# Kernel tuning notes

Measured on AMD Instinct MI355X. Metric: run time of the kernel, lower is better.

The kernel has to match this reference:

```python
import jax, jax.numpy as jnp
import numpy as np

L, B, T, D, H, FF = 4, 8, 1024, 256, 8, 1024
DK = D // H
SCALE = 1.0 / np.sqrt(DK)


def _ln(x, g, b, eps=1e-6):
    m = jnp.mean(x, axis=-1, keepdims=True)
    v = jnp.mean(jnp.square(x - m), axis=-1, keepdims=True)
    return (x - m) * jax.lax.rsqrt(v + eps) * g + b


def _l2norm(x, eps=1e-8):
    n = jnp.sqrt(jnp.sum(jnp.square(x), axis=-1, keepdims=True))
    return x / jnp.maximum(n, eps)


def setup_inputs() -> dict:
    key = jax.random.key(0)
    ks = jax.random.split(key, 8)
    s = 0.02
    inp = {
        'x': jax.random.normal(ks[0], (B, T, D), dtype=jnp.float32),
        'padding_mask': jnp.zeros((B, T), dtype=bool),
        'ln1_g': jnp.ones((L, D), jnp.float32), 'ln1_b': jnp.zeros((L, D), jnp.float32),
        'qn_g': jnp.ones((L, D), jnp.float32), 'qn_b': jnp.zeros((L, D), jnp.float32),
        'Wqkv': jax.random.normal(ks[1], (L, 3 * D, D), jnp.float32) * s,
        'bqkv': jnp.zeros((L, 3 * D), jnp.float32),
        'Wo': jax.random.normal(ks[2], (L, D, D), jnp.float32) * s,
        'bo': jnp.zeros((L, D), jnp.float32),
        'ln2_g': jnp.ones((L, D), jnp.float32), 'ln2_b': jnp.zeros((L, D), jnp.float32),
        'W1': jax.random.normal(ks[3], (L, FF, D), jnp.float32) * s,
        'b1': jnp.zeros((L, FF), jnp.float32),
        'W2': jax.random.normal(ks[4], (L, D, FF), jnp.float32) * s,
        'b2': jnp.zeros((L, D), jnp.float32),
        'alpha': jnp.full((L,), 0.1, jnp.float32),
        'beta': jnp.full((L,), 0.1, jnp.float32),
    }
    return inp


def _block(x, pad_mask, p):
    (g1, bb1, qg, qb, wqkv, bqkv, wo, bo, g2, bb2, w1, b1, w2, b2, a, be) = p
    Bn, Tn, Dn = x.shape
    # --- SemiCausalAttention on norm1(x) ---
    xn = _ln(x, g1, bb1)
    h = _ln(xn, qg, qb)                      # q_norm LayerNorm
    qkv = h @ wqkv.T + bqkv                  # [B,T,3D]
    qkv = qkv.reshape(Bn, Tn, 3, H, DK).transpose(2, 0, 3, 1, 4)  # [3,B,H,T,dk]
    Q, K, V = qkv[0], qkv[1], qkv[2]
    Q = _l2norm(Q)
    K = _l2norm(K)
    scores = jnp.einsum('bhtd,bhsd->bhts', Q, K) * SCALE
    scores = jnp.clip(scores, -10.0, 10.0)
    causal = jnp.triu(jnp.ones((Tn, Tn), dtype=bool), k=1)        # True = future
    scores = jnp.where(causal[None, None], -10000.0, scores)
    scores = jnp.where(pad_mask[:, None, None, :], -10000.0, scores)
    attn = jax.nn.softmax(scores, axis=-1)
    ao = jnp.einsum('bhts,bhsd->bhtd', attn, V)                   # [B,H,T,dk]
    ao = ao.transpose(0, 2, 1, 3).reshape(Bn, Tn, Dn)
    attn_out = (ao @ wo.T + bo) * 0.5
    x = x + jnp.tanh(a) * attn_out
    # --- FFN ---
    f = _ln(x, g2, bb2)
    f = jax.nn.gelu(f @ w1.T + b1, approximate=False)
    f = f @ w2.T + b2
    x = x + jnp.tanh(be) * f
    return jnp.clip(x, -100.0, 100.0)


def reference(x, padding_mask, ln1_g, ln1_b, qn_g, qn_b, Wqkv, bqkv, Wo, bo,
              ln2_g, ln2_b, W1, b1, W2, b2, alpha, beta):
    params = (ln1_g, ln1_b, qn_g, qn_b, Wqkv, bqkv, Wo, bo,
              ln2_g, ln2_b, W1, b1, W2, b2, alpha, beta)

    def step(carry, p):
        return _block(carry, padding_mask, p), None

    out, _ = jax.lax.scan(step, x, params)
    return out
```

## Files before the change

kernel.cpp:

```cpp
#include <hip/hip_runtime.h>
#include <hip/hip_bf16.h>
#include <math.h>

#define BB 8
#define TT 1024
#define DD 256
#define HH 8
#define BT 8192

typedef __attribute__((ext_vector_type(4))) float f32x4;
typedef __attribute__((ext_vector_type(16))) float f32x16;
typedef __attribute__((ext_vector_type(8))) short short8;
typedef __attribute__((ext_vector_type(4))) short short4v;
typedef __attribute__((ext_vector_type(8))) __bf16 bf16x8;

__device__ inline float bf2f(short s) {
  unsigned int u = ((unsigned int)(unsigned short)s) << 16;
  return __builtin_bit_cast(float, u);
}
__device__ inline short f2bf(float f) {
  unsigned int u = __builtin_bit_cast(unsigned int, f);
  unsigned int lsb = (u >> 16) & 1u;
  u += 0x7fffu + lsb;
  return (short)(u >> 16);
}
__device__ inline unsigned int cvtpk(float lo, float hi) {
  unsigned int r;
  asm("v_cvt_pk_bf16_f32 %0, %1, %2" : "=v"(r) : "v"(lo), "v"(hi));
  return r;
}

__device__ inline f32x4 mfma16(short8 a, short8 b, f32x4 c) {
  return __builtin_amdgcn_mfma_f32_16x16x32_bf16(
      __builtin_bit_cast(bf16x8, a), __builtin_bit_cast(bf16x8, b), c, 0, 0, 0);
}
__device__ inline f32x16 mfma32(short8 a, short8 b, f32x16 c) {
  return __builtin_amdgcn_mfma_f32_32x32x16_bf16(
      __builtin_bit_cast(bf16x8, a), __builtin_bit_cast(bf16x8, b), c, 0, 0, 0);
}

__device__ inline void gload_lds16(void* lds, const void* g) {
  __builtin_amdgcn_global_load_lds(
      (const __attribute__((address_space(1))) unsigned int*)g,
      (__attribute__((address_space(3))) unsigned int*)lds, 16, 0, 0);
}

__global__ __launch_bounds__(256) void cvt_all(
    const float4* __restrict__ s0, short4v* __restrict__ d0, int n0,
    const float4* __restrict__ s1, short4v* __restrict__ d1, int n1,
    const float4* __restrict__ s2, short4v* __restrict__ d2, int n2,
    const float4* __restrict__ s3, short4v* __restrict__ d3, int n3)
{
  int i = blockIdx.x * 256 + threadIdx.x;
  const float4* s; short4v* d;
  if (i < n0) { s = s0 + i; d = d0 + i; }
  else if ((i -= n0) < n1) { s = s1 + i; d = d1 + i; }
  else if ((i -= n1) < n2) { s = s2 + i; d = d2 + i; }
  else if ((i -= n2) < n3) { s = s3 + i; d = d3 + i; }
  else return;
  float4 v = *s;
  short4v o;
  o[0] = f2bf(v.x); o[1] = f2bf(v.y); o[2] = f2bf(v.z); o[3] = f2bf(v.w);
  *d = o;
}

__global__ __launch_bounds__(256) void ln_kernel(
    const float* __restrict__ Xin,
    const float* __restrict__ g1, const float* __restrict__ b1,
    const float* __restrict__ g2, const float* __restrict__ b2,
    short* __restrict__ out)
{
  const int row = blockIdx.x * 4 + (threadIdx.x >> 6);
  const int lane = threadIdx.x & 63;
  const float4 v = *(const float4*)(Xin + (size_t)row * 256 + lane * 4);
  float y[4] = {v.x, v.y, v.z, v.w};

  float s = y[0] + y[1] + y[2] + y[3];
  #pragma unroll
  for (int m = 32; m >= 1; m >>= 1) s += __shfl_xor(s, m, 64);
  float mean = s * (1.0f / 256.0f);
  float sq = 0.f;
  #pragma unroll
  for (int i = 0; i < 4; ++i) { y[i] -= mean; sq += y[i] * y[i]; }
  #pragma unroll
  for (int m = 32; m >= 1; m >>= 1) sq += __shfl_xor(sq, m, 64);
  float rs = rsqrtf(sq * (1.0f / 256.0f) + 1e-6f);
  #pragma unroll
  for (int i = 0; i < 4; ++i) y[i] = y[i] * rs * g1[lane * 4 + i] + b1[lane * 4 + i];

  float s2 = y[0] + y[1] + y[2] + y[3];
  #pragma unroll
  for (int m = 32; m >= 1; m >>= 1) s2 += __shfl_xor(s2, m, 64);
  float m2 = s2 * (1.0f / 256.0f);
  float sq2 = 0.f;
  #pragma unroll
  for (int i = 0; i < 4; ++i) { y[i] -= m2; sq2 += y[i] * y[i]; }
  #pragma unroll
  for (int m = 32; m >= 1; m >>= 1) sq2 += __shfl_xor(sq2, m, 64);
  float rs2 = rsqrtf(sq2 * (1.0f / 256.0f) + 1e-6f);
  #pragma unroll
  for (int i = 0; i < 4; ++i) y[i] = y[i] * rs2 * g2[lane * 4 + i] + b2[lane * 4 + i];

  #pragma unroll
  for (int i = 0; i < 4; ++i) out[(size_t)row * 256 + lane * 4 + i] = f2bf(y[i]);
}

template<int BN, int EPI>
__global__ __launch_bounds__(256) void gemm_bt(
    const short* __restrict__ A, const short* __restrict__ Bw,
    const float* __restrict__ bias,
    short* __restrict__ O0, short* __restrict__ O1, short* __restrict__ O2,
    int M, int N, int K)
{
  constexpr int MI = (BN == 128) ? 4 : 2;
  __shared__ __align__(16) short A_s[2][128 * 64];
  __shared__ __align__(16) short B_s[2][BN * 64];
  const int tid = threadIdx.x;
  const int lane = tid & 63;
  const int w = tid >> 6;
  const int lo4 = lane & 15, hi2 = lane >> 4;
  int wm, wn0;
  if (BN == 128) { wm = (w >> 1) * 64; wn0 = (w & 1) * 64; }
  else           { wm = w * 32;        wn0 = 0; }
  const int bid = blockIdx.x + blockIdx.y * gridDim.x;
  const int nwg = gridDim.x * gridDim.y;
  const int wg = (bid & 7) * (nwg >> 3) + (bid >> 3);
  const int tM = (wg / gridDim.x) * 128, tN = (wg % gridDim.x) * BN;

  f32x4 acc[MI][4];
  #pragma unroll
  for (int i = 0; i < MI; ++i)
    #pragma unroll
    for (int j = 0; j < 4; ++j) acc[i][j] = (f32x4){0.f, 0.f, 0.f, 0.f};

  auto stage = [&](int buf, int k0) {
    #pragma unroll
    for (int ri = 0; ri < 4; ++ri) {
      int o = ri * 2048 + tid * 8;
      int row = o >> 6;
      int col = (o & 63) ^ ((row & 7) << 3);
      gload_lds16(&A_s[buf][ri * 2048 + w * 512], A + (size_t)(tM + row) * K + k0 + col);
    }
    #pragma unroll
    for (int ri = 0; ri < BN / 32; ++ri) {
      int o = ri * 2048 + tid * 8;
      int row = o >> 6;
      int col = (o & 63) ^ ((row & 7) << 3);
      gload_lds16(&B_s[buf][ri * 2048 + w * 512], Bw + (size_t)(tN + row) * K + k0 + col);
    }
  };

  const int nt = K >> 6;
  stage(0, 0);
  __syncthreads();
  for (int t = 0; t < nt; ++t) {
    const int cur = t & 1;
    if (t + 1 < nt) stage(cur ^ 1, (t + 1) << 6);
    #pragma unroll
    for (int kc = 0; kc < 2; ++kc) {
      short8 af[MI], bfr[4];
      #pragma unroll
      for (int i = 0; i < MI; ++i) {
        int row = wm + i * 16 + lo4;
        af[i] = *(const short8*)&A_s[cur][row * 64 + ((kc * 32 + hi2 * 8) ^ ((row & 7) << 3))];
      }
      #pragma unroll
      for (int j = 0; j < 4; ++j) {
        int row = wn0 + j * 16 + lo4;
        bfr[j] = *(const short8*)&B_s[cur][row * 64 + ((kc * 32 + hi2 * 8) ^ ((row & 7) << 3))];
      }
      #pragma unroll
      for (int i = 0; i < MI; ++i)
        #pragma unroll
        for (int j = 0; j < 4; ++j)
          acc[i][j] = mfma16(af[i], bfr[j], acc[i][j]);
    }
    __syncthreads();
  }

  if (EPI == 4) {
    #pragma unroll
    for (int i = 0; i < MI; ++i)
      #pragma unroll
      for (int j = 0; j < 4; ++j)
        #pragma unroll
        for (int r = 0; r < 4; ++r)
          acc[i][j][r] += bias[tN + wn0 + j * 16 + lo4];
    if (tN >= 512) {
      #pragma unroll
      for (int i = 0; i < MI; ++i) {
        #pragma unroll
        for (int j = 0; j < 4; ++j) {
          short4v o;
          #pragma unroll
          for (int r = 0; r < 4; ++r) o[r] = f2bf(acc[i][j][r]);
          int row0 = tM + wm + i * 16 + hi2 * 4;
          int colr = (tN + wn0 + j * 16 + lo4) - 512;
          int h = colr >> 5, d = colr & 31;
          int b = row0 >> 10, t0 = row0 & 1023;
          *(short4v*)(O2 + (((size_t)(b * 8 + h) * 32 + d) << 10) + t0) = o;
        }
      }
      return;
    }
    {
      const float C2 = 0.25503489702966368f;
      const float sc = (tN < 256) ? C2 : 1.0f;
      #pragma unroll
      for (int i = 0; i < MI; ++i) {
        #pragma unroll
        for (int r = 0; r < 4; ++r) {
          float s01 = acc[i][0][r] * acc[i][0][r] + acc[i][1][r] * acc[i][1][r];
          float s23 = acc[i][2][r] * acc[i][2][r] + acc[i][3][r] * acc[i][3][r];
          #pragma unroll
          for (int m = 1; m <= 8; m <<= 1) {
            s01 += __shfl_xor(s01, m, 64);
            s23 += __shfl_xor(s23, m, 64);
          }
          float n01 = sc / fmaxf(sqrtf(s01), 1e-8f);
          float n23 = sc / fmaxf(sqrtf(s23), 1e-8f);
          acc[i][0][r] *= n01; acc[i][1][r] *= n01;
          acc[i][2][r] *= n23; acc[i][3][r] *= n23;
        }
      }
    }
    short* dst = (tN < 256) ? O0 : O1;
    #pragma unroll
    for (int i = 0; i < MI; ++i)
      #pragma unroll
      for (int j = 0; j < 4; ++j)
        #pragma unroll
        for (int r = 0; r < 4; ++r) {
          int row = tM + wm + i * 16 + hi2 * 4 + r;
          int colr = (tN + wn0 + j * 16 + lo4) & 255;
          int h = colr >> 5, d = colr & 31;
          size_t idx = (((size_t)((row >> 10) * 8 + h) << 10) | (size_t)(row & 1023)) * 32 + d;
          dst[idx] = f2bf(acc[i][j][r]);
        }
    return;
  }

  #pragma unroll
  for (int i = 0; i < MI; ++i) {
    #pragma unroll
    for (int j = 0; j < 4; ++j) {
      #pragma unroll
      for (int r = 0; r < 4; ++r) {
        int row = tM + wm + i * 16 + hi2 * 4 + r;
        int col = tN + wn0 + j * 16 + lo4;
        float v = acc[i][j][r] + bias[col];
        size_t idx = (size_t)row * N + col;
        if (EPI == 2) {
          float t1 = v * v;
          float arg = fminf(v * (1.0f + 0.044715f * t1) * 2.3022077f, 80.0f);
          float ex;
          asm("v_exp_f32 %0, %1" : "=v"(ex) : "v"(arg));
          float gl = v * ex * __builtin_amdgcn_rcpf(ex + 1.0f);
          O0[idx] = f2bf(gl);
        } else {
          O0[idx] = f2bf(v);
        }
      }
    }
  }
}

template<int MODE>
__global__ __launch_bounds__(256) void gemm_ln(
    const short* __restrict__ A, const short* __restrict__ Bw,
    const float* __restrict__ bias, const float* Xin, float* X,
    short* __restrict__ Obf, const float* __restrict__ scale_p,
    const float* __restrict__ gA, const float* __restrict__ bA,
    const float* __restrict__ gB, const float* __restrict__ bB,
    int K, int doLN)
{
  __shared__ __align__(16) short A_s[2][32 * 64];
  __shared__ __align__(16) short B_s[2][256 * 64];
  __shared__ float Red[2][32][4][2];
  const int tid = threadIdx.x;
  const int lane = tid & 63;
  const int w = tid >> 6;
  const int lo4 = lane & 15, hi2 = lane >> 4;
  const int tM = blockIdx.x * 32;

  f32x4 acc[2][4];
  #pragma unroll
  for (int i = 0; i < 2; ++i)
    #pragma unroll
    for (int j = 0; j < 4; ++j) acc[i][j] = (f32x4){0.f, 0.f, 0.f, 0.f};

  auto stage = [&](int buf, int k0) {
    {
      int o = tid * 8;
      int row = o >> 6;
      int col = (o & 63) ^ ((row & 7) << 3);
      gload_lds16(&A_s[buf][w * 512], A + (size_t)(tM + row) * K + k0 + col);
    }
    #pragma unroll
    for (int ri = 0; ri < 8; ++ri) {
      int o = ri * 2048 + tid * 8;
      int row = o >> 6;
      int col = (o & 63) ^ ((row & 7) << 3);
      gload_lds16(&B_s[buf][ri * 2048 + w * 512], Bw + (size_t)row * K + k0 + col);
    }
  };

  const int nt = K >> 6;
  stage(0, 0);
  __syncthreads();
  for (int t = 0; t < nt; ++t) {
    const int cur = t & 1;
    if (t + 1 < nt) stage(cur ^ 1, (t + 1) << 6);
    #pragma unroll
    for (int kc = 0; kc < 2; ++kc) {
      short8 af[2], bfr[4];
      #pragma unroll
      for (int i = 0; i < 2; ++i) {
        int row = i * 16 + lo4;
        af[i] = *(const short8*)&A_s[cur][row * 64 + ((kc * 32 + hi2 * 8) ^ ((row & 7) << 3))];
      }
      #pragma unroll
      for (int j = 0; j < 4; ++j) {
        int row = w * 64 + j * 16 + lo4;
        bfr[j] = *(const short8*)&B_s[cur][row * 64 + ((kc * 32 + hi2 * 8) ^ ((row & 7) << 3))];
      }
      #pragma unroll
      for (int i = 0; i < 2; ++i)
        #pragma unroll
        for (int j = 0; j < 4; ++j)
          acc[i][j] = mfma16(af[i], bfr[j], acc[i][j]);
    }
    __syncthreads();
  }

  const float ts = tanhf(scale_p[0]);
  float xv[2][4][4];
  #pragma unroll
  for (int i = 0; i < 2; ++i)
    #pragma unroll
    for (int j = 0; j < 4; ++j)
      #pragma unroll
      for (int r = 0; r < 4; ++r) {
        int row = i * 16 + hi2 * 4 + r;
        int col = w * 64 + j * 16 + lo4;
        float v = acc[i][j][r] + bias[col];
        size_t idx = (size_t)(tM + row) * 256 + col;
        float xn;
        if (MODE == 0) {
          xn = Xin[idx] + ts * 0.5f * v;
        } else {
          xn = X[idx] + ts * v;
          xn = fminf(100.f, fmaxf(-100.f, xn));
        }
        X[idx] = xn;
        xv[i][j][r] = xn;
      }

  if (!doLN) return;

  #pragma unroll
  for (int i = 0; i < 2; ++i)
    #pragma unroll
    for (int r = 0; r < 4; ++r) {
      float s = xv[i][0][r] + xv[i][1][r] + xv[i][2][r] + xv[i][3][r];
      float q = xv[i][0][r] * xv[i][0][r] + xv[i][1][r] * xv[i][1][r]
              + xv[i][2][r] * xv[i][2][r] + xv[i][3][r] * xv[i][3][r];
      #pragma unroll
      for (int m = 1; m <= 8; m <<= 1) { s += __shfl_xor(s, m, 64); q += __shfl_xor(q, m, 64); }
      if (lo4 == 0) { Red[0][i * 16 + hi2 * 4 + r][w][0] = s; Red[0][i * 16 + hi2 * 4 + r][w][1] = q; }
    }
  __syncthreads();
  #pragma unroll
  for (int i = 0; i < 2; ++i)
    #pragma unroll
    for (int r = 0; r < 4; ++r) {
      int row = i * 16 + hi2 * 4 + r;
      float s = Red[0][row][0][0] + Red[0][row][1][0] + Red[0][row][2][0] + Red[0][row][3][0];
      float q = Red[0][row][0][1] + Red[0][row][1][1] + Red[0][row][2][1] + Red[0][row][3][1];
      float mu = s * (1.0f / 256.0f);
      float var = q * (1.0f / 256.0f) - mu * mu;
      float rs = rsqrtf(var + 1e-6f);
      #pragma unroll
      for (int j = 0; j < 4; ++j) {
        int col = w * 64 + j * 16 + lo4;
        xv[i][j][r] = (xv[i][j][r] - mu) * rs * gA[col] + bA[col];
      }
    }

  if (MODE == 1) {
    #pragma unroll
    for (int i = 0; i < 2; ++i)
      #pragma unroll
      for (int r = 0; r < 4; ++r) {
        float s = xv[i][0][r] + xv[i][1][r] + xv[i][2][r] + xv[i][3][r];
        float q = xv[i][0][r] * xv[i][0][r] + xv[i][1][r] * xv[i][1][r]
                + xv[i][2][r] * xv[i][2][r] + xv[i][3][r] * xv[i][3][r];
        #pragma unroll
        for (int m = 1; m <= 8; m <<= 1) { s += __shfl_xor(s, m, 64); q += __shfl_xor(q, m, 64); }
        if (lo4 == 0) { Red[1][i * 16 + hi2 * 4 + r][w][0] = s; Red[1][i * 16 + hi2 * 4 + r][w][1] = q; }
      }
    __syncthreads();
    #pragma unroll
    for (int i = 0; i < 2; ++i)
      #pragma unroll
      for (int r = 0; r < 4; ++r) {
        int row = i * 16 + hi2 * 4 + r;
        float s = Red[1][row][0][0] + Red[1][row][1][0] + Red[1][row][2][0] + Red[1][row][3][0];
        float q = Red[1][row][0][1] + Red[1][row][1][1] + Red[1][row][2][1] + Red[1][row][3][1];
        float mu = s * (1.0f / 256.0f);
        float var = q * (1.0f / 256.0f) - mu * mu;
        float rs = rsqrtf(var + 1e-6f);
        #pragma unroll
        for (int j = 0; j < 4; ++j) {
          int col = w * 64 + j * 16 + lo4;
          xv[i][j][r] = (xv[i][j][r] - mu) * rs * gB[col] + bB[col];
        }
      }
  }

  #pragma unroll
  for (int i = 0; i < 2; ++i)
    #pragma unroll
    for (int j = 0; j < 4; ++j)
      #pragma unroll
      for (int r = 0; r < 4; ++r) {
        int row = i * 16 + hi2 * 4 + r;
        int col = w * 64 + j * 16 + lo4;
        Obf[(size_t)(tM + row) * 256 + col] = f2bf(xv[i][j][r]);
      }
}

__device__ __forceinline__ void pv_acc(const unsigned int* PKO, int half_,
                                       short8 vb, int hi1, f32x16& acc) {
  unsigned int keep0 = hi1 ? PKO[4 * half_ + 2] : PKO[4 * half_ + 0];
  unsigned int keep1 = hi1 ? PKO[4 * half_ + 3] : PKO[4 * half_ + 1];
  unsigned int send0 = hi1 ? PKO[4 * half_ + 0] : PKO[4 * half_ + 2];
  unsigned int send1 = hi1 ? PKO[4 * half_ + 1] : PKO[4 * half_ + 3];
  unsigned int r0 = (unsigned int)__shfl_xor((int)send0, 32, 64);
  unsigned int r1 = (unsigned int)__shfl_xor((int)send1, 32, 64);
  union { unsigned int u[4]; short8 s; } fa;
  fa.u[0] = hi1 ? r0 : keep0;
  fa.u[1] = hi1 ? r1 : keep1;
  fa.u[2] = hi1 ? keep0 : r0;
  fa.u[3] = hi1 ? keep1 : r1;
  acc = mfma32(fa.s, vb, acc);
}

template<bool KG1, bool M0, bool M1>
__device__ __forceinline__ void attn_tile(
    int t, const short* __restrict__ Kbase, const short* __restrict__ VTl,
    const short8* qb, unsigned int pm0, unsigned int pm1, int lo5, int hi1,
    f32x16& oaccA, f32x16& oaccB, float& rsum)
{
  const short* kp0 = Kbase + (size_t)(t * 64 + lo5) * 32;
  short8 k00 = *(const short8*)(kp0 + hi1 * 8);
  short8 k01 = *(const short8*)(kp0 + 16 + hi1 * 8);
  short8 k10, k11;
  if (KG1) {
    const short* kp1 = Kbase + (size_t)(t * 64 + 32 + lo5) * 32;
    k10 = *(const short8*)(kp1 + hi1 * 8);
    k11 = *(const short8*)(kp1 + 16 + hi1 * 8);
  }
  const short* vp = VTl + t * 64 + hi1 * 8;
  short8 vb0 = *(const short8*)(vp);
  short8 vb1 = *(const short8*)(vp + 16);
  short8 vb2, vb3;
  if (KG1) {
    vb2 = *(const short8*)(vp + 32);
    vb3 = *(const short8*)(vp + 48);
  }
  unsigned int pk0[8], pk1[8];
  {
    f32x16 z = (f32x16)0.0f;
    z = mfma32(k00, qb[0], z);
    z = mfma32(k01, qb[1], z);
    float pr[16];
    #pragma unroll
    for (int r = 0; r < 16; ++r) {
      float sv = __builtin_amdgcn_fmed3f(z[r], -14.4269504f, 14.4269504f);
      float pe;
      asm("v_exp_f32 %0, %1" : "=v"(pe) : "v"(sv));
      const int keyrel = (r & 3) + 8 * (r >> 2) + 4 * hi1;
      if (M0) pe = (keyrel > lo5) ? 0.f : pe;
      if (pm0) pe = ((pm0 >> keyrel) & 1u) ? 0.f : pe;
      pr[r] = pe;
      rsum += pe;
    }
    #pragma unroll
    for (int i = 0; i < 8; ++i) pk0[i] = cvtpk(pr[2 * i], pr[2 * i + 1]);
  }
  if (KG1) {
    f32x16 z = (f32x16)0.0f;
    z = mfma32(k10, qb[0], z);
    z = mfma32(k11, qb[1], z);
    float pr[16];
    #pragma unroll
    for (int r = 0; r < 16; ++r) {
      float sv = __builtin_amdgcn_fmed3f(z[r], -14.4269504f, 14.4269504f);
      float pe;
      asm("v_exp_f32 %0, %1" : "=v"(pe) : "v"(sv));
      const int keyrel = (r & 3) + 8 * (r >> 2) + 4 * hi1;
      if (M1) pe = (keyrel > lo5) ? 0.f : pe;
      if (pm1) pe = ((pm1 >> keyrel) & 1u) ? 0.f : pe;
      pr[r] = pe;
      rsum += pe;
    }
    #pragma unroll
    for (int i = 0; i < 8; ++i) pk1[i] = cvtpk(pr[2 * i], pr[2 * i + 1]);
  }
  pv_acc(pk0, 0, vb0, hi1, oaccA);
  pv_acc(pk0, 1, vb1, hi1, oaccB);
  if (KG1) {
    pv_acc(pk1, 0, vb2, hi1, oaccA);
    pv_acc(pk1, 1, vb3, hi1, oaccB);
  }
}

__global__ __launch_bounds__(256, 2) void attn_kernel(
    const short* __restrict__ Qp, const short* __restrict__ Kp,
    const short* __restrict__ vT, const unsigned char* __restrict__ pad,
    short* __restrict__ ao)
{
  __shared__ float Red[2][17][64];
  const int tid = threadIdx.x, lane = tid & 63, w = tid >> 6;
  const int lo5 = lane & 31, hi1 = lane >> 5;
  const int bid = blockIdx.x;
  const int b = bid & 7;
  const int h = (bid >> 3) & 7;
  const int bj = bid >> 6;
  const int p = w >> 1;
  const int half = w & 1;
  const int j = p ? (31 - bj) : bj;
  const size_t rowbase = (size_t)b * TT;
  const int bh = b * 8 + h;
  const int qrow = j * 32 + lo5;
  const int ntile = (j >> 1) + 1;

  const short* Kbase = Kp + ((size_t)bh << 10) * 32;
  const short* VTl = vT + ((size_t)bh * 32 + lo5) * 1024;

  const ulonglong2 pv = *(const ulonglong2*)(pad + rowbase + lane * 16);
  const unsigned long long anyp = __ballot((pv.x | pv.y) != 0ull);

  short8 qb[2];
  #pragma unroll
  for (int c2 = 0; c2 < 2; ++c2)
    qb[c2] = *(const short8*)(Qp + (((size_t)bh << 10) + qrow) * 32 + c2 * 16 + hi1 * 8);

  f32x16 oaccA = (f32x16)0.0f;
  f32x16 oaccB = (f32x16)0.0f;
  float rsum = 0.f;

  for (int t = half; t < ntile; t += 2) {
    unsigned long long pm = 0;
    if ((anyp >> (4 * t)) & 0xFull)
      pm = __ballot(pad[rowbase + t * 64 + lane] != 0);
    unsigned int pm0 = (unsigned int)pm, pm1 = (unsigned int)(pm >> 32);
    if (t + 1 < ntile)
      attn_tile<true, false, false>(t, Kbase, VTl, qb, pm0, pm1, lo5, hi1, oaccA, oaccB, rsum);
    else if (j & 1)
      attn_tile<true, false, true>(t, Kbase, VTl, qb, pm0, pm1, lo5, hi1, oaccA, oaccB, rsum);
    else
      attn_tile<false, true, false>(t, Kbase, VTl, qb, pm0, pm1, lo5, hi1, oaccA, oaccB, rsum);
  }

  if (half) {
    #pragma unroll
    for (int r = 0; r < 16; ++r) Red[p][r][lane] = oaccA[r] + oaccB[r];
    Red[p][16][lane] = rsum;
  }
  __syncthreads();
  if (!half) {
    #pragma unroll
    for (int r = 0; r < 16; ++r) oaccA[r] += oaccB[r] + Red[p][r][lane];
    rsum += Red[p][16][lane];
    rsum += __shfl_xor(rsum, 32, 64);
    float rinv = 1.0f / fmaxf(rsum, 1e-30f);
    #pragma unroll
    for (int r = 0; r < 16; ++r) {
      int ql = (r & 3) + 8 * (r >> 2) + 4 * hi1;
      float riv = __shfl(rinv, ql, 64);
      int qg = j * 32 + ql;
      ao[(rowbase + qg) * 256 + h * 32 + lo5] = f2bf(oaccA[r] * riv);
    }
  }
}

extern "C" void kernel_launch(void* const* d_in, const int* in_sizes, int n_in,
                              void* d_out, int out_size, void* d_ws, size_t ws_size,
                              hipStream_t stream) {
  const float* x_in  = (const float*)d_in[0];
  const unsigned char* pad = (const unsigned char*)d_in[1];
  const float* ln1_g = (const float*)d_in[2];
  const float* ln1_b = (const float*)d_in[3];
  const float* qn_g  = (const float*)d_in[4];
  const float* qn_b  = (const float*)d_in[5];
  const float* Wqkv  = (const float*)d_in[6];
  const float* bqkv  = (const float*)d_in[7];
  const float* Wo    = (const float*)d_in[8];
  const float* bo    = (const float*)d_in[9];
  const float* ln2_g = (const float*)d_in[10];
  const float* ln2_b = (const float*)d_in[11];
  const float* W1    = (const float*)d_in[12];
  const float* b1    = (const float*)d_in[13];
  const float* W2    = (const float*)d_in[14];
  const float* b2    = (const float*)d_in[15];
  const float* alpha = (const float*)d_in[16];
  const float* beta  = (const float*)d_in[17];

  char* ws = (char*)d_ws;
  size_t off = 0;
  short* wqkv_bf = (short*)(ws + off); off += (size_t)4 * 768 * 256 * 2;
  short* wo_bf   = (short*)(ws + off); off += (size_t)4 * 256 * 256 * 2;
  short* w1_bf   = (short*)(ws + off); off += (size_t)4 * 1024 * 256 * 2;
  short* w2_bf   = (short*)(ws + off); off += (size_t)4 * 256 * 1024 * 2;
  short* h_bf    = (short*)(ws + off); off += (size_t)BT * 256 * 2;
  short* Qp_bf   = (short*)(ws + off); off += (size_t)BT * 256 * 2;
  short* Kp_bf   = (short*)(ws + off); off += (size_t)BT * 256 * 2;
  short* vT_bf   = (short*)(ws + off); off += (size_t)BT * 256 * 2;
  short* ao_bf   = (short*)(ws + off); off += (size_t)BT * 256 * 2;
  short* g_bf    = (short*)(ws + off); off += (size_t)BT * 1024 * 2;

  float* X = (float*)d_out;

  cvt_all<<<3072, 256, 0, stream>>>(
      (const float4*)Wqkv, (short4v*)wqkv_bf, 4 * 768 * 256 / 4,
      (const float4*)Wo,   (short4v*)wo_bf,   4 * 256 * 256 / 4,
      (const float4*)W1,   (short4v*)w1_bf,   4 * 1024 * 256 / 4,
      (const float4*)W2,   (short4v*)w2_bf,   4 * 256 * 1024 / 4);

  ln_kernel<<<2048, 256, 0, stream>>>(x_in, ln1_g, ln1_b, qn_g, qn_b, h_bf);

  for (int l = 0; l < 4; ++l) {
    gemm_bt<128, 4><<<dim3(6, 64), 256, 0, stream>>>(h_bf, wqkv_bf + (size_t)l * 768 * 256,
                                                     bqkv + l * 768, Qp_bf, Kp_bf, vT_bf,
                                                     8192, 768, 256);
    attn_kernel<<<1024, 256, 0, stream>>>(Qp_bf, Kp_bf, vT_bf, pad, ao_bf);
    gemm_ln<0><<<256, 256, 0, stream>>>(ao_bf, wo_bf + (size_t)l * 256 * 256,
                                        bo + l * 256, (l == 0) ? x_in : (const float*)X, X,
                                        h_bf, alpha + l,
                                        ln2_g + l * 256, ln2_b + l * 256,
                                        nullptr, nullptr, 256, 1);
    gemm_bt<128, 2><<<dim3(8, 64), 256, 0, stream>>>(h_bf, w1_bf + (size_t)l * 1024 * 256,
                                                     b1 + l * 1024, g_bf, nullptr, nullptr,
                                                     8192, 1024, 256);
    const int nl = (l < 3) ? (l + 1) : 0;
    gemm_ln<1><<<256, 256, 0, stream>>>(g_bf, w2_bf + (size_t)l * 256 * 1024,
                                        b2 + l * 256, X, X, h_bf, beta + l,
                                        ln1_g + nl * 256, ln1_b + nl * 256,
                                        qn_g + nl * 256, qn_b + nl * 256,
                                        1024, (l < 3) ? 1 : 0);
  }
}
```

Before: 348.8 us.

## Use 512-thread blocks in gemm_ln and smaller N-tiles for QKV GEMM

The fused GEMM+LayerNorm kernel now runs 8 waves per block, each owning 32 output columns instead of 64. Staging loads and the cross-wave reduction buffers are resized to match, and an extra barrier guards reuse of the reduction array. The QKV GEMM switches to a 64-wide tile with twice as many blocks. Both changes aim to put more waves on the 256-CU device, since the row-tiled kernels launch only 256 blocks, at the cost of more cross-wave reduction traffic and less reuse per wave.

```diff
diff --git a/kernel.cpp b/kernel.cpp
--- a/kernel.cpp
+++ b/kernel.cpp
@@ -266,7 +266,7 @@
 }
 
 template<int MODE>
-__global__ __launch_bounds__(256) void gemm_ln(
+__global__ __launch_bounds__(512) void gemm_ln(
     const short* __restrict__ A, const short* __restrict__ Bw,
     const float* __restrict__ bias, const float* Xin, float* X,
     short* __restrict__ Obf, const float* __restrict__ scale_p,
@@ -276,32 +276,33 @@
 {
   __shared__ __align__(16) short A_s[2][32 * 64];
   __shared__ __align__(16) short B_s[2][256 * 64];
-  __shared__ float Red[2][32][4][2];
+  __shared__ float Red[2][32][8][2];
   const int tid = threadIdx.x;
   const int lane = tid & 63;
   const int w = tid >> 6;
   const int lo4 = lane & 15, hi2 = lane >> 4;
   const int tM = blockIdx.x * 32;
-
-  f32x4 acc[2][4];
+  const int wn0 = w * 32;
+
+  f32x4 acc[2][2];
   #pragma unroll
   for (int i = 0; i < 2; ++i)
     #pragma unroll
-    for (int j = 0; j < 4; ++j) acc[i][j] = (f32x4){0.f, 0.f, 0.f, 0.f};
+    for (int j = 0; j < 2; ++j) acc[i][j] = (f32x4){0.f, 0.f, 0.f, 0.f};
 
   auto stage = [&](int buf, int k0) {
-    {
+    if (tid < 256) {
       int o = tid * 8;
       int row = o >> 6;
       int col = (o & 63) ^ ((row & 7) << 3);
       gload_lds16(&A_s[buf][w * 512], A + (size_t)(tM + row) * K + k0 + col);
     }
     #pragma unroll
-    for (int ri = 0; ri < 8; ++ri) {
-      int o = ri * 2048 + tid * 8;
+    for (int ri = 0; ri < 4; ++ri) {
+      int o = ri * 4096 + tid * 8;
       int row = o >> 6;
       int col = (o & 63) ^ ((row & 7) << 3);
-      gload_lds16(&B_s[buf][ri * 2048 + w * 512], Bw + (size_t)row * K + k0 + col);
+      gload_lds16(&B_s[buf][ri * 4096 + w * 512], Bw + (size_t)row * K + k0 + col);
     }
   };
 
@@ -313,36 +314,36 @@
     if (t + 1 < nt) stage(cur ^ 1, (t + 1) << 6);
     #pragma unroll
     for (int kc = 0; kc < 2; ++kc) {
-      short8 af[2], bfr[4];
+      short8 af[2], bfr[2];
       #pragma unroll
       for (int i = 0; i < 2; ++i) {
         int row = i * 16 + lo4;
         af[i] = *(const short8*)&A_s[cur][row * 64 + ((kc * 32 + hi2 * 8) ^ ((row & 7) << 3))];
       }
       #pragma unroll
-      for (int j = 0; j < 4; ++j) {
-        int row = w * 64 + j * 16 + lo4;
+      for (int j = 0; j < 2; ++j) {
+        int row = wn0 + j * 16 + lo4;
         bfr[j] = *(const short8*)&B_s[cur][row * 64 + ((kc * 32 + hi2 * 8) ^ ((row & 7) << 3))];
       }
       #pragma unroll
       for (int i = 0; i < 2; ++i)
         #pragma unroll
-        for (int j = 0; j < 4; ++j)
+        for (int j = 0; j < 2; ++j)
           acc[i][j] = mfma16(af[i], bfr[j], acc[i][j]);
     }
     __syncthreads();
   }
 
   const float ts = tanhf(scale_p[0]);
-  float xv[2][4][4];
+  float xv[2][2][4];
   #pragma unroll
   for (int i = 0; i < 2; ++i)
     #pragma unroll
-    for (int j = 0; j < 4; ++j)
+    for (int j = 0; j < 2; ++j)
       #pragma unroll
       for (int r = 0; r < 4; ++r) {
         int row = i * 16 + hi2 * 4 + r;
-        int col = w * 64 + j * 16 + lo4;
+        int col = wn0 + j * 16 + lo4;
         float v = acc[i][j][r] + bias[col];
         size_t idx = (size_t)(tM + row) * 256 + col;
         float xn;
@@ -362,9 +363,8 @@
   for (int i = 0; i < 2; ++i)
     #pragma unroll
     for (int r = 0; r < 4; ++r) {
-      float s = xv[i][0][r] + xv[i][1][r] + xv[i][2][r] + xv[i][3][r];
-      float q = xv[i][0][r] * xv[i][0][r] + xv[i][1][r] * xv[i][1][r]
-              + xv[i][2][r] * xv[i][2][r] + xv[i][3][r] * xv[i][3][r];
+      float s = xv[i][0][r] + xv[i][1][r];
+      float q = xv[i][0][r] * xv[i][0][r] + xv[i][1][r] * xv[i][1][r];
       #pragma unroll
       for (int m = 1; m <= 8; m <<= 1) { s += __shfl_xor(s, m, 64); q += __shfl_xor(q, m, 64); }
       if (lo4 == 0) { Red[0][i * 16 + hi2 * 4 + r][w][0] = s; Red[0][i * 16 + hi2 * 4 + r][w][1] = q; }
@@ -375,26 +375,27 @@
     #pragma unroll
     for (int r = 0; r < 4; ++r) {
       int row = i * 16 + hi2 * 4 + r;
-      float s = Red[0][row][0][0] + Red[0][row][1][0] + Red[0][row][2][0] + Red[0][row][3][0];
-      float q = Red[0][row][0][1] + Red[0][row][1][1] + Red[0][row][2][1] + Red[0][row][3][1];
+      float s = 0.f, q = 0.f;
+      #pragma unroll
+      for (int ww = 0; ww < 8; ++ww) { s += Red[0][row][ww][0]; q += Red[0][row][ww][1]; }
       float mu = s * (1.0f / 256.0f);
       float var = q * (1.0f / 256.0f) - mu * mu;
       float rs = rsqrtf(var + 1e-6f);
       #pragma unroll
-      for (int j = 0; j < 4; ++j) {
-        int col = w * 64 + j * 16 + lo4;
+      for (int j = 0; j < 2; ++j) {
+        int col = wn0 + j * 16 + lo4;
         xv[i][j][r] = (xv[i][j][r] - mu) * rs * gA[col] + bA[col];
       }
     }
 
   if (MODE == 1) {
+    __syncthreads();
     #pragma unroll
     for (int i = 0; i < 2; ++i)
       #pragma unroll
       for (int r = 0; r < 4; ++r) {
-        float s = xv[i][0][r] + xv[i][1][r] + xv[i][2][r] + xv[i][3][r];
-        float q = xv[i][0][r] * xv[i][0][r] + xv[i][1][r] * xv[i][1][r]
-                + xv[i][2][r] * xv[i][2][r] + xv[i][3][r] * xv[i][3][r];
+        float s = xv[i][0][r] + xv[i][1][r];
+        float q = xv[i][0][r] * xv[i][0][r] + xv[i][1][r] * xv[i][1][r];
         #pragma unroll
         for (int m = 1; m <= 8; m <<= 1) { s += __shfl_xor(s, m, 64); q += __shfl_xor(q, m, 64); }
         if (lo4 == 0) { Red[1][i * 16 + hi2 * 4 + r][w][0] = s; Red[1][i * 16 + hi2 * 4 + r][w][1] = q; }
@@ -405,14 +406,15 @@
       #pragma unroll
       for (int r = 0; r < 4; ++r) {
         int row = i * 16 + hi2 * 4 + r;
-        float s = Red[1][row][0][0] + Red[1][row][1][0] + Red[1][row][2][0] + Red[1][row][3][0];
-        float q = Red[1][row][0][1] + Red[1][row][1][1] + Red[1][row][2][1] + Red[1][row][3][1];
+        float s = 0.f, q = 0.f;
+        #pragma unroll
+        for (int ww = 0; ww < 8; ++ww) { s += Red[1][row][ww][0]; q += Red[1][row][ww][1]; }
         float mu = s * (1.0f / 256.0f);
         float var = q * (1.0f / 256.0f) - mu * mu;
         float rs = rsqrtf(var + 1e-6f);
         #pragma unroll
-        for (int j = 0; j < 4; ++j) {
-          int col = w * 64 + j * 16 + lo4;
+        for (int j = 0; j < 2; ++j) {
+          int col = wn0 + j * 16 + lo4;
           xv[i][j][r] = (xv[i][j][r] - mu) * rs * gB[col] + bB[col];
         }
       }
@@ -421,11 +423,11 @@
   #pragma unroll
   for (int i = 0; i < 2; ++i)
     #pragma unroll
-    for (int j = 0; j < 4; ++j)
+    for (int j = 0; j < 2; ++j)
       #pragma unroll
       for (int r = 0; r < 4; ++r) {
         int row = i * 16 + hi2 * 4 + r;
-        int col = w * 64 + j * 16 + lo4;
+        int col = wn0 + j * 16 + lo4;
         Obf[(size_t)(tM + row) * 256 + col] = f2bf(xv[i][j][r]);
       }
 }
@@ -632,11 +634,11 @@
   ln_kernel<<<2048, 256, 0, stream>>>(x_in, ln1_g, ln1_b, qn_g, qn_b, h_bf);
 
   for (int l = 0; l < 4; ++l) {
-    gemm_bt<128, 4><<<dim3(6, 64), 256, 0, stream>>>(h_bf, wqkv_bf + (size_t)l * 768 * 256,
+    gemm_bt<64, 4><<<dim3(12, 64), 256, 0, stream>>>(h_bf, wqkv_bf + (size_t)l * 768 * 256,
                                                      bqkv + l * 768, Qp_bf, Kp_bf, vT_bf,
                                                      8192, 768, 256);
     attn_kernel<<<1024, 256, 0, stream>>>(Qp_bf, Kp_bf, vT_bf, pad, ao_bf);
-    gemm_ln<0><<<256, 256, 0, stream>>>(ao_bf, wo_bf + (size_t)l * 256 * 256,
+    gemm_ln<0><<<256, 512, 0, stream>>>(ao_bf, wo_bf + (size_t)l * 256 * 256,
                                         bo + l * 256, (l == 0) ? x_in : (const float*)X, X,
                                         h_bf, alpha + l,
                                         ln2_g + l * 256, ln2_b + l * 256,
@@ -645,7 +647,7 @@
                                                      b1 + l * 1024, g_bf, nullptr, nullptr,
                                                      8192, 1024, 256);
     const int nl = (l < 3) ? (l + 1) : 0;
-    gemm_ln<1><<<256, 256, 0, stream>>>(g_bf, w2_bf + (size_t)l * 256 * 1024,
+    gemm_ln<1><<<256, 512, 0, stream>>>(g_bf, w2_bf + (size_t)l * 256 * 1024,
                                         b2 + l * 256, X, X, h_bf, beta + l,
                                         ln1_g + nl * 256, ln1_b + nl * 256,
                                         qn_g + nl * 256, qn_b + nl * 256,
```

After: 327.2 us (median of 3 runs). 6.2% less time.
